# Kernel optimization log

Measured on AMD Instinct MI355X. Metric: run time of the kernel, lower is better.

## Reference

```python
import jax, jax.numpy as jnp
import numpy as np

D_MODEL = 1024
NUM_HEADS = 16
HEAD_DIM = D_MODEL // NUM_HEADS  # 64
ROPE_BASE = 10000.0


def _rope_tables(n_pos, dim):
    # 1D rotary tables for `dim` channels (rotate-half convention).
    inv_freq = 1.0 / (ROPE_BASE ** (jnp.arange(0, dim, 2, dtype=jnp.float32) / dim))
    ang = jnp.arange(n_pos, dtype=jnp.float32)[:, None] * inv_freq[None, :]  # (P, dim/2)
    cos = jnp.concatenate([jnp.cos(ang), jnp.cos(ang)], axis=-1)  # (P, dim)
    sin = jnp.concatenate([jnp.sin(ang), jnp.sin(ang)], axis=-1)
    return cos, sin


def _rotate_half(v):
    v1, v2 = jnp.split(v, 2, axis=-1)
    return jnp.concatenate([-v2, v1], axis=-1)


def rope_2d(x, H, W):
    # x: (N, H, W, nh, hd). First half of hd rotated by row index, second by col index.
    d_half = HEAD_DIM // 2
    x_h, x_w = x[..., :d_half], x[..., d_half:]
    cos_h, sin_h = _rope_tables(H, d_half)  # (H, d_half)
    cos_w, sin_w = _rope_tables(W, d_half)  # (W, d_half)
    cos_h = cos_h[None, :, None, None, :]
    sin_h = sin_h[None, :, None, None, :]
    cos_w = cos_w[None, None, :, None, :]
    sin_w = sin_w[None, None, :, None, :]
    x_h = x_h * cos_h + _rotate_half(x_h) * sin_h
    x_w = x_w * cos_w + _rotate_half(x_w) * sin_w
    return jnp.concatenate([x_h, x_w], axis=-1)


def setup_inputs() -> dict:
    key = jax.random.key(0)
    k_x, k_qkv, k_p, k_b = jax.random.split(key, 4)
    B, T, H, W = 4, 32, 16, 16
    x = jax.random.normal(k_x, (B, T, H, W, D_MODEL), dtype=jnp.float32)
    w_qkv = jax.random.normal(k_qkv, (D_MODEL, 3 * D_MODEL), dtype=jnp.float32) * 0.02
    w_proj = jax.random.normal(k_p, (D_MODEL, D_MODEL), dtype=jnp.float32) * 0.02
    b_proj = jax.random.normal(k_b, (D_MODEL,), dtype=jnp.float32) * 0.02
    return {"x": x, "w_qkv": w_qkv, "w_proj": w_proj, "b_proj": b_proj}


def reference(x, w_qkv, w_proj, b_proj):
    B, T, H, W, C = x.shape
    N, S = B * T, H * W
    scale = HEAD_DIM ** -0.5
    xf = x.reshape(N, S, C)
    qkv = xf @ w_qkv  # (N, S, 3C)  [qkv_bias=False]
    q, k, v = jnp.split(qkv, 3, axis=-1)
    q = q.reshape(N, H, W, NUM_HEADS, HEAD_DIM)
    k = k.reshape(N, H, W, NUM_HEADS, HEAD_DIM)
    v = v.reshape(N, S, NUM_HEADS, HEAD_DIM)
    q = rope_2d(q, H, W).reshape(N, S, NUM_HEADS, HEAD_DIM)
    k = rope_2d(k, H, W).reshape(N, S, NUM_HEADS, HEAD_DIM)
    attn = jnp.einsum('nshd,nthd->nhst', q, k) * scale  # (N, nh, S, S)
    attn = jax.nn.softmax(attn, axis=-1)  # attn_drop=0.0
    out = jnp.einsum('nhst,nthd->nshd', attn, v).reshape(N, S, C)
    out = out @ w_proj + b_proj
    return out.reshape(B, T, H, W, C)
```

## Files before the change

kernel.cpp:

```cpp
#include <hip/hip_runtime.h>
#include <hip/hip_bf16.h>
#include <stdint.h>

typedef __attribute__((ext_vector_type(8))) short bf16x8;
typedef __attribute__((ext_vector_type(4))) float f32x4;
typedef __attribute__((ext_vector_type(4))) unsigned short ushort4_t;

__device__ __forceinline__ unsigned short f2bf(float f) {
  union { float f; unsigned int i; } x; x.f = f;
  return (unsigned short)((x.i + 0x7fffu + ((x.i >> 16) & 1u)) >> 16);
}

__device__ __forceinline__ void gl_lds16(const void* g, void* l) {
  __builtin_amdgcn_global_load_lds(
      (const __attribute__((address_space(1))) unsigned int*)(uintptr_t)g,
      (__attribute__((address_space(3))) unsigned int*)(uint32_t)(uintptr_t)l,
      16, 0, 0);
}

__device__ __forceinline__ void bar() {
  asm volatile("" ::: "memory");
  __builtin_amdgcn_s_barrier();
  asm volatile("" ::: "memory");
}

__constant__ float INVF[16] = {
  1.0f,   0.56234132519f,  0.31622776601f,  0.17782794100f,
  0.1f,   0.056234132519f, 0.031622776601f, 0.017782794100f,
  0.01f,  0.0056234132519f,0.0031622776601f,0.0017782794100f,
  0.001f, 0.00056234132519f,0.00031622776601f,0.00017782794100f
};

__global__ __launch_bounds__(256) void k_conv_x(const float4* __restrict__ src,
                                                ushort4_t* __restrict__ dst, int n4) {
  int i = blockIdx.x * 256 + threadIdx.x;
  if (i < n4) {
    float4 v = src[i];
    ushort4_t r = { f2bf(v.x), f2bf(v.y), f2bf(v.z), f2bf(v.w) };
    dst[i] = r;
  }
}

__global__ __launch_bounds__(256) void k_transpose_bf16(const float* __restrict__ src,
                                                        unsigned short* __restrict__ dst,
                                                        int R, int C) {
  __shared__ unsigned short tile[64][65];
  const int bj = blockIdx.x, bi = blockIdx.y;
  const int t = threadIdx.x, lr = t >> 6, lc = t & 63;
  #pragma unroll
  for (int i = 0; i < 16; i++) {
    int r = i * 4 + lr;
    tile[r][lc] = f2bf(src[(size_t)(bi * 64 + r) * C + bj * 64 + lc]);
  }
  __syncthreads();
  #pragma unroll
  for (int i = 0; i < 16; i++) {
    int r = i * 4 + lr;
    dst[(size_t)(bj * 64 + r) * R + bi * 64 + lc] = tile[lc][r];
  }
}

template<int F32OUT, int ROPE>
__global__ __launch_bounds__(512, 2) void k_gemm_bt(
    const unsigned short* __restrict__ A, const unsigned short* __restrict__ B,
    unsigned short* __restrict__ Cb, float* __restrict__ Cf,
    const float* __restrict__ bias, int M, int N, int K) {
  __shared__ __align__(16) unsigned short As[2 * 256 * 64];
  __shared__ __align__(16) unsigned short Bs[2 * 256 * 64];
  const int tid = threadIdx.x;
  const int lane = tid & 63, wid = tid >> 6;
  const int cl = lane & 15, gr = lane >> 4;
  const int wm = wid >> 2, wn = wid & 3;
  const int l8 = lane >> 3, l7 = lane & 7;
  const int mBase = blockIdx.y * 256, nBase = blockIdx.x * 256;
  const int KT = K >> 6;
  const int ldsW = (wid * 8) * 64;

  const unsigned short* aP[4];
  const unsigned short* bP[4];
  #pragma unroll
  for (int i = 0; i < 4; i++) {
    aP[i] = A + (size_t)(mBase + i * 64 + wid * 8 + l8) * K + (l7 ^ l8) * 8;
    bP[i] = B + (size_t)(nBase + i * 64 + wid * 8 + l8) * K + (l7 ^ l8) * 8;
  }

  const f32x4 zero4 = {0.f, 0.f, 0.f, 0.f};
  f32x4 acc[8][4];
  #pragma unroll
  for (int a = 0; a < 8; a++)
    #pragma unroll
    for (int b = 0; b < 4; b++) acc[a][b] = zero4;

  #pragma unroll
  for (int i = 0; i < 4; i++) gl_lds16(aP[i], &As[(i * 64) * 64 + ldsW]);
  #pragma unroll
  for (int i = 0; i < 4; i++) gl_lds16(bP[i], &Bs[(i * 64) * 64 + ldsW]);
  #pragma unroll
  for (int i = 0; i < 4; i++) gl_lds16(aP[i] + 64, &As[16384 + (i * 64) * 64 + ldsW]);
  #pragma unroll
  for (int i = 0; i < 4; i++) gl_lds16(bP[i] + 64, &Bs[16384 + (i * 64) * 64 + ldsW]);
  asm volatile("s_waitcnt vmcnt(8)" ::: "memory");
  bar();

  for (int c = 0; c < KT; ++c) {
    const int s = c & 1;
    const unsigned short* as_ = As + s * 16384;
    const unsigned short* bs_ = Bs + s * 16384;

    if (c + 1 < KT) {
      const int koff = (c + 1) * 64;
      const int so = (s ^ 1) * 16384;
      #pragma unroll
      for (int i = 0; i < 4; i++) gl_lds16(aP[i] + koff, &As[so + (i * 64) * 64 + ldsW]);
      #pragma unroll
      for (int i = 0; i < 4; i++) gl_lds16(bP[i] + koff, &Bs[so + (i * 64) * 64 + ldsW]);
    }

    #pragma unroll
    for (int kc = 0; kc < 2; ++kc) {
      const int coff = ((kc * 4 + gr) ^ (cl & 7)) * 8;
      bf16x8 bv[4];
      #pragma unroll
      for (int nt = 0; nt < 4; nt++)
        bv[nt] = *(const bf16x8*)&bs_[(wn * 64 + nt * 16 + cl) * 64 + coff];
      #pragma unroll
      for (int h = 0; h < 2; ++h) {
        bf16x8 af[4];
        #pragma unroll
        for (int t = 0; t < 4; t++)
          af[t] = *(const bf16x8*)&as_[(wm * 128 + h * 64 + t * 16 + cl) * 64 + coff];
        __builtin_amdgcn_s_setprio(1);
        #pragma unroll
        for (int mt = 0; mt < 4; mt++)
          #pragma unroll
          for (int nt = 0; nt < 4; nt++)
            acc[h * 4 + mt][nt] =
                __builtin_amdgcn_mfma_f32_16x16x32_bf16(af[mt], bv[nt], acc[h * 4 + mt][nt], 0, 0, 0);
        __builtin_amdgcn_s_setprio(0);
      }
    }

    if (c + 1 < KT) {
      asm volatile("s_waitcnt vmcnt(0)" ::: "memory");
      bar();
    }
  }

  if (ROPE && nBase < 2048) {
    const float f = INVF[cl];
    #pragma unroll
    for (int amt = 0; amt < 8; amt++)
      #pragma unroll
      for (int r = 0; r < 4; r++) {
        const int sp = (mBase + wm * 128 + amt * 16 + gr * 4 + r) & 255;
        float sh, ch, sw, cw;
        __sincosf((float)(sp >> 4) * f, &sh, &ch);
        __sincosf((float)(sp & 15) * f, &sw, &cw);
        const float a = acc[amt][0][r], b = acc[amt][1][r];
        const float cc = acc[amt][2][r], d = acc[amt][3][r];
        acc[amt][0][r] = a * ch - b * sh;
        acc[amt][1][r] = b * ch + a * sh;
        acc[amt][2][r] = cc * cw - d * sw;
        acc[amt][3][r] = d * cw + cc * sw;
      }
  }

  #pragma unroll
  for (int amt = 0; amt < 8; amt++)
    #pragma unroll
    for (int nt = 0; nt < 4; nt++)
      #pragma unroll
      for (int r = 0; r < 4; r++) {
        const int row = mBase + wm * 128 + amt * 16 + gr * 4 + r;
        const int col = nBase + wn * 64 + nt * 16 + cl;
        const float v = acc[amt][nt][r];
        if (F32OUT) Cf[(size_t)row * N + col] = v + bias[col];
        else        Cb[(size_t)row * N + col] = f2bf(v);
      }
}

__global__ __launch_bounds__(256, 3) void k_attn(const unsigned short* __restrict__ qkv,
                                                 unsigned short* __restrict__ attn_out) {
  __shared__ __align__(16) unsigned short Qp[4][64 * 64];
  __shared__ __align__(16) unsigned short Kt[64 * 64];
  __shared__ __align__(16) unsigned short Vt[64 * 64];
  const int blk = blockIdx.x;
  const int n = blk >> 4, h = blk & 15;
  const int tid = threadIdx.x;
  const int lane = tid & 63, wid = tid >> 6;
  const int cl = lane & 15, gr = lane >> 4;
  const int l8 = lane >> 3, l7 = lane & 7;
  const unsigned short* qbase = qkv + (size_t)n * 256 * 3072 + h * 64;
  const unsigned short* kbase = qbase + 1024;
  const unsigned short* vbase = qbase + 2048;

  #pragma unroll
  for (int i = 0; i < 8; i++)
    gl_lds16(qbase + (size_t)(wid * 64 + i * 8 + l8) * 3072 + (l7 ^ l8) * 8,
             &Qp[wid][i * 8 * 64]);
  #pragma unroll
  for (int i = 0; i < 2; i++) {
    const int r0 = (wid * 2 + i) * 8;
    gl_lds16(kbase + (size_t)(r0 + l8) * 3072 + (l7 ^ l8) * 8, &Kt[r0 * 64]);
  }

  unsigned int vr[2][4];
  #pragma unroll
  for (int i = 0; i < 2; i++) {
    const int u = i * 256 + tid;
    const int t0 = u >> 5, d = (u & 31) * 2;
    #pragma unroll
    for (int k = 0; k < 4; k++)
      vr[i][k] = *(const unsigned int*)(vbase + (size_t)(t0 + 16 * k) * 3072 + d);
  }
  __syncthreads();

  bf16x8 qf[4][2];
  #pragma unroll
  for (int mt = 0; mt < 4; mt++)
    #pragma unroll
    for (int kc = 0; kc < 2; kc++)
      qf[mt][kc] = *(const bf16x8*)&Qp[wid][(mt * 16 + cl) * 64 + ((kc * 4 + gr) ^ (cl & 7)) * 8];

  const f32x4 zero4 = {0.f, 0.f, 0.f, 0.f};
  f32x4 o[4][4];
  float lsum[4][4];
  #pragma unroll
  for (int a = 0; a < 4; a++)
    #pragma unroll
    for (int b = 0; b < 4; b++) { o[a][b] = zero4; lsum[a][b] = 0.f; }

  for (int tc = 0; tc < 4; tc++) {
    #pragma unroll
    for (int i = 0; i < 2; i++) {
      const int u = i * 256 + tid;
      const int t0 = u >> 5, d = (u & 31) * 2;
      const unsigned int r0 = vr[i][0], r1 = vr[i][1], r2 = vr[i][2], r3 = vr[i][3];
      uint2 lo, hi;
      lo.x = (r0 & 0xffffu) | (r1 << 16);
      lo.y = (r2 & 0xffffu) | (r3 << 16);
      hi.x = (r0 >> 16) | (r1 & 0xffff0000u);
      hi.y = (r2 >> 16) | (r3 & 0xffff0000u);
      *(uint2*)&Vt[d * 64 + ((t0 >> 1) ^ (d & 7)) * 8 + (t0 & 1) * 4] = lo;
      const int d1 = d + 1;
      *(uint2*)&Vt[d1 * 64 + ((t0 >> 1) ^ (d1 & 7)) * 8 + (t0 & 1) * 4] = hi;
    }
    if (tc < 3) {
      #pragma unroll
      for (int i = 0; i < 2; i++) {
        const int u = i * 256 + tid;
        const int t0 = u >> 5, d = (u & 31) * 2;
        #pragma unroll
        for (int k = 0; k < 4; k++)
          vr[i][k] = *(const unsigned int*)(vbase + (size_t)((tc + 1) * 64 + t0 + 16 * k) * 3072 + d);
      }
    }

    #pragma unroll
    for (int mt = 0; mt < 4; mt++) {
      f32x4 sacc[4] = {zero4, zero4, zero4, zero4};
      #pragma unroll
      for (int kc = 0; kc < 2; kc++)
        #pragma unroll
        for (int nt = 0; nt < 4; nt++) {
          const bf16x8 kf = *(const bf16x8*)&Kt[(nt * 16 + cl) * 64 + ((kc * 4 + gr) ^ (cl & 7)) * 8];
          sacc[nt] = __builtin_amdgcn_mfma_f32_16x16x32_bf16(qf[mt][kc], kf, sacc[nt], 0, 0, 0);
        }
      #pragma unroll
      for (int r = 0; r < 4; r++) {
        const float p0 = __expf(sacc[0][r] * 0.125f);
        const float p1 = __expf(sacc[1][r] * 0.125f);
        const float p2 = __expf(sacc[2][r] * 0.125f);
        const float p3 = __expf(sacc[3][r] * 0.125f);
        lsum[mt][r] += (p0 + p1) + (p2 + p3);
        float2 f01; f01.x = p0; f01.y = p1;
        float2 f23; f23.x = p2; f23.y = p3;
        __hip_bfloat162 b01 = __float22bfloat162_rn(f01);
        __hip_bfloat162 b23 = __float22bfloat162_rn(f23);
        union { __hip_bfloat162 h; unsigned int u; } c0, c1;
        c0.h = b01; c1.h = b23;
        uint2 w; w.x = c0.u; w.y = c1.u;
        const int m = mt * 16 + gr * 4 + r;
        *(uint2*)&Qp[wid][m * 64 + ((cl >> 1) ^ (m & 7)) * 8 + (cl & 1) * 4] = w;
      }
    }
    __syncthreads();

    if (tc < 3) {
      #pragma unroll
      for (int i = 0; i < 2; i++) {
        const int r0 = (wid * 2 + i) * 8;
        gl_lds16(kbase + (size_t)((tc + 1) * 64 + r0 + l8) * 3072 + (l7 ^ l8) * 8, &Kt[r0 * 64]);
      }
    }

    #pragma unroll
    for (int kc = 0; kc < 2; kc++) {
      bf16x8 vf[4], pf[4];
      #pragma unroll
      for (int dt = 0; dt < 4; dt++)
        vf[dt] = *(const bf16x8*)&Vt[(dt * 16 + cl) * 64 + ((kc * 4 + gr) ^ (cl & 7)) * 8];
      #pragma unroll
      for (int mt = 0; mt < 4; mt++)
        pf[mt] = *(const bf16x8*)&Qp[wid][(mt * 16 + cl) * 64 + ((kc * 4 + gr) ^ (cl & 7)) * 8];
      #pragma unroll
      for (int mt = 0; mt < 4; mt++)
        #pragma unroll
        for (int dt = 0; dt < 4; dt++)
          o[mt][dt] = __builtin_amdgcn_mfma_f32_16x16x32_bf16(pf[mt], vf[dt], o[mt][dt], 0, 0, 0);
    }
    __syncthreads();
  }

  #pragma unroll
  for (int mt = 0; mt < 4; mt++)
    #pragma unroll
    for (int r = 0; r < 4; r++) {
      float l = lsum[mt][r];
      l += __shfl_xor(l, 1);
      l += __shfl_xor(l, 2);
      l += __shfl_xor(l, 4);
      l += __shfl_xor(l, 8);
      const float inv = 1.0f / l;
      const int srow = wid * 64 + mt * 16 + gr * 4 + r;
      #pragma unroll
      for (int dt = 0; dt < 4; dt++)
        attn_out[(size_t)(n * 256 + srow) * 1024 + h * 64 + dt * 16 + cl] =
            f2bf(o[mt][dt][r] * inv);
    }
}

extern "C" void kernel_launch(void* const* d_in, const int* in_sizes, int n_in,
                              void* d_out, int out_size, void* d_ws, size_t ws_size,
                              hipStream_t stream) {
  const float* x      = (const float*)d_in[0];
  const float* w_qkv  = (const float*)d_in[1];
  const float* w_proj = (const float*)d_in[2];
  const float* b_proj = (const float*)d_in[3];
  float* out = (float*)d_out;
  char* ws = (char*)d_ws;

  unsigned short* x_bf    = (unsigned short*)ws;
  unsigned short* wqkvT   = (unsigned short*)(ws + 67108864);
  unsigned short* wprojT  = (unsigned short*)(ws + 73400320);
  unsigned short* qkvb    = (unsigned short*)(ws + 75497472);
  unsigned short* attn_bf = x_bf;

  k_conv_x<<<32768, 256, 0, stream>>>((const float4*)x, (ushort4_t*)x_bf, 8388608);
  k_transpose_bf16<<<dim3(48, 16), 256, 0, stream>>>(w_qkv, wqkvT, 1024, 3072);
  k_transpose_bf16<<<dim3(16, 16), 256, 0, stream>>>(w_proj, wprojT, 1024, 1024);

  k_gemm_bt<0, 1><<<dim3(12, 128), 512, 0, stream>>>(x_bf, wqkvT, qkvb, nullptr, nullptr,
                                                     32768, 3072, 1024);
  k_attn<<<2048, 256, 0, stream>>>(qkvb, attn_bf);

  k_gemm_bt<1, 0><<<dim3(4, 128), 512, 0, stream>>>(attn_bf, wprojT, nullptr, out, b_proj,
                                                    32768, 1024, 1024);
}
```

Measured before the change: 657.2 us.

## Restructure GEMM main loop into quadrant-staged ping-pong pipeline with XCD-aware block remap

```diff
diff --git a/kernel.cpp b/kernel.cpp
--- a/kernel.cpp
+++ b/kernel.cpp
@@ -59,6 +59,55 @@
     dst[(size_t)(bj * 64 + r) * R + bi * 64 + lc] = tile[lc][r];
   }
 }
+
+
+#define LDA(dst, base, hm)                                                      \
+  do {                                                                          \
+    _Pragma("unroll") for (int t_ = 0; t_ < 4; t_++) {                          \
+      dst[0][t_] = *(const bf16x8*)&base[(wm * 128 + (hm) * 64 + t_ * 16 + cl) * 64 + cf0]; \
+      dst[1][t_] = *(const bf16x8*)&base[(wm * 128 + (hm) * 64 + t_ * 16 + cl) * 64 + cf1]; \
+    }                                                                           \
+  } while (0)
+
+#define LDB(dst, base, hn)                                                      \
+  do {                                                                          \
+    _Pragma("unroll") for (int u_ = 0; u_ < 2; u_++) {                          \
+      dst[0][u_] = *(const bf16x8*)&base[(wn * 64 + (hn) * 32 + u_ * 16 + cl) * 64 + cf0]; \
+      dst[1][u_] = *(const bf16x8*)&base[(wn * 64 + (hn) * 32 + u_ * 16 + cl) * 64 + cf1]; \
+    }                                                                           \
+  } while (0)
+
+#define MFMA_Q(hm, hn, AFR, BVR)                                                \
+  do {                                                                          \
+    __builtin_amdgcn_s_setprio(1);                                              \
+    _Pragma("unroll") for (int kc_ = 0; kc_ < 2; kc_++)                         \
+      _Pragma("unroll") for (int mt_ = 0; mt_ < 4; mt_++)                       \
+        _Pragma("unroll") for (int u_ = 0; u_ < 2; u_++)                        \
+          acc[(hm) * 4 + mt_][(hn) * 2 + u_] =                                  \
+              __builtin_amdgcn_mfma_f32_16x16x32_bf16(                          \
+                  AFR[kc_][mt_], BVR[kc_][u_],                                  \
+                  acc[(hm) * 4 + mt_][(hn) * 2 + u_], 0, 0, 0);                 \
+    __builtin_amdgcn_s_setprio(0);                                              \
+  } while (0)
+
+#define STAGE_A(tile_, half_)                                                   \
+  do {                                                                          \
+    const int so_ = ((tile_) & 1) * 16384;                                      \
+    const int ko_ = (tile_) * 64;                                               \
+    gl_lds16(aP[(half_) * 2] + ko_,     &As[so_ + ((half_) * 2) * 4096 + ldsW]);     \
+    gl_lds16(aP[(half_) * 2 + 1] + ko_, &As[so_ + ((half_) * 2 + 1) * 4096 + ldsW]); \
+  } while (0)
+
+#define STAGE_B(tile_, half_)                                                   \
+  do {                                                                          \
+    const int so_ = ((tile_) & 1) * 16384;                                      \
+    const int ko_ = (tile_) * 64;                                               \
+    gl_lds16(bP[(half_) * 2] + ko_,     &Bs[so_ + ((half_) * 2) * 4096 + ldsW]);     \
+    gl_lds16(bP[(half_) * 2 + 1] + ko_, &Bs[so_ + ((half_) * 2 + 1) * 4096 + ldsW]); \
+  } while (0)
+
+#define LGKM0() asm volatile("s_waitcnt lgkmcnt(0)" ::: "memory")
+#define VMC(n)  asm volatile("s_waitcnt vmcnt(" #n ")" ::: "memory")
 
 template<int F32OUT, int ROPE>
 __global__ __launch_bounds__(512, 2) void k_gemm_bt(
@@ -72,9 +121,19 @@
   const int cl = lane & 15, gr = lane >> 4;
   const int wm = wid >> 2, wn = wid & 3;
   const int l8 = lane >> 3, l7 = lane & 7;
-  const int mBase = blockIdx.y * 256, nBase = blockIdx.x * 256;
+
+  const int gx = gridDim.x;
+  const int nwg = gx * gridDim.y;
+  const int fb = blockIdx.y * gx + blockIdx.x;
+  const int q = nwg >> 3;
+  const int nid = (fb & 7) * q + (fb >> 3);
+  const int bx = nid % gx, by = nid / gx;
+  const int mBase = by * 256, nBase = bx * 256;
+
   const int KT = K >> 6;
   const int ldsW = (wid * 8) * 64;
+  const int cf0 = ((0 * 4 + gr) ^ (cl & 7)) * 8;
+  const int cf1 = ((1 * 4 + gr) ^ (cl & 7)) * 8;
 
   const unsigned short* aP[4];
   const unsigned short* bP[4];
@@ -91,71 +150,74 @@
     #pragma unroll
     for (int b = 0; b < 4; b++) acc[a][b] = zero4;
 
-  #pragma unroll
-  for (int i = 0; i < 4; i++) gl_lds16(aP[i], &As[(i * 64) * 64 + ldsW]);
-  #pragma unroll
-  for (int i = 0; i < 4; i++) gl_lds16(bP[i], &Bs[(i * 64) * 64 + ldsW]);
-  #pragma unroll
-  for (int i = 0; i < 4; i++) gl_lds16(aP[i] + 64, &As[16384 + (i * 64) * 64 + ldsW]);
-  #pragma unroll
-  for (int i = 0; i < 4; i++) gl_lds16(bP[i] + 64, &Bs[16384 + (i * 64) * 64 + ldsW]);
-  asm volatile("s_waitcnt vmcnt(8)" ::: "memory");
+  STAGE_A(0, 0); STAGE_A(0, 1); STAGE_B(0, 0); STAGE_B(0, 1);
+  STAGE_B(1, 0); STAGE_B(1, 1);
+  VMC(4);
   bar();
 
-  for (int c = 0; c < KT; ++c) {
-    const int s = c & 1;
-    const unsigned short* as_ = As + s * 16384;
-    const unsigned short* bs_ = Bs + s * 16384;
-
-    if (c + 1 < KT) {
-      const int koff = (c + 1) * 64;
-      const int so = (s ^ 1) * 16384;
-      #pragma unroll
-      for (int i = 0; i < 4; i++) gl_lds16(aP[i] + koff, &As[so + (i * 64) * 64 + ldsW]);
-      #pragma unroll
-      for (int i = 0; i < 4; i++) gl_lds16(bP[i] + koff, &Bs[so + (i * 64) * 64 + ldsW]);
-    }
-
-    #pragma unroll
-    for (int kc = 0; kc < 2; ++kc) {
-      const int coff = ((kc * 4 + gr) ^ (cl & 7)) * 8;
-      bf16x8 bv[4];
-      #pragma unroll
-      for (int nt = 0; nt < 4; nt++)
-        bv[nt] = *(const bf16x8*)&bs_[(wn * 64 + nt * 16 + cl) * 64 + coff];
-      #pragma unroll
-      for (int h = 0; h < 2; ++h) {
-        bf16x8 af[4];
-        #pragma unroll
-        for (int t = 0; t < 4; t++)
-          af[t] = *(const bf16x8*)&as_[(wm * 128 + h * 64 + t * 16 + cl) * 64 + coff];
-        __builtin_amdgcn_s_setprio(1);
-        #pragma unroll
-        for (int mt = 0; mt < 4; mt++)
-          #pragma unroll
-          for (int nt = 0; nt < 4; nt++)
-            acc[h * 4 + mt][nt] =
-                __builtin_amdgcn_mfma_f32_16x16x32_bf16(af[mt], bv[nt], acc[h * 4 + mt][nt], 0, 0, 0);
-        __builtin_amdgcn_s_setprio(0);
-      }
-    }
-
-    if (c + 1 < KT) {
-      asm volatile("s_waitcnt vmcnt(0)" ::: "memory");
-      bar();
-    }
+  bf16x8 af[2][4], bva[2][2], bvb[2][2];
+
+  for (int c = 0; c < KT; c += 2) {
+    const unsigned short* a0 = As;
+    const unsigned short* b0 = Bs;
+    const unsigned short* a1 = As + 16384;
+    const unsigned short* b1 = Bs + 16384;
+    const int c2 = c + 2, c3 = c + 3;
+
+    LDA(af, a0, 0); LDB(bva, b0, 0);
+    STAGE_A(c + 1, 0);
+    asm volatile("s_waitcnt lgkmcnt(8)" ::: "memory");
+    bar(); LGKM0();
+    MFMA_Q(0, 0, af, bva);
+    bar();
+    LDB(bvb, b0, 1);
+    STAGE_A(c + 1, 1);
+    bar(); LGKM0();
+    MFMA_Q(0, 1, af, bvb);
+    bar();
+    LDA(af, a0, 1);
+    if (c2 < KT) STAGE_B(c2, 0);
+    bar(); LGKM0();
+    MFMA_Q(1, 1, af, bvb);
+    bar();
+    if (c2 < KT) { STAGE_B(c2, 1); VMC(4); } else { VMC(0); }
+    bar();
+    MFMA_Q(1, 0, af, bva);
+    bar();
+
+    LDA(af, a1, 0); LDB(bva, b1, 0);
+    if (c2 < KT) STAGE_A(c2, 0);
+    asm volatile("s_waitcnt lgkmcnt(8)" ::: "memory");
+    bar(); LGKM0();
+    MFMA_Q(0, 0, af, bva);
+    bar();
+    LDB(bvb, b1, 1);
+    if (c2 < KT) STAGE_A(c2, 1);
+    bar(); LGKM0();
+    MFMA_Q(0, 1, af, bvb);
+    bar();
+    LDA(af, a1, 1);
+    if (c3 < KT) STAGE_B(c3, 0);
+    bar(); LGKM0();
+    MFMA_Q(1, 1, af, bvb);
+    bar();
+    if (c3 < KT)      { STAGE_B(c3, 1); VMC(4); }
+    else if (c2 < KT) { VMC(0); }
+    bar();
+    MFMA_Q(1, 0, af, bva);
+    if (c2 < KT) bar();
   }
 
   if (ROPE && nBase < 2048) {
-    const float f = INVF[cl];
+    const float f2 = INVF[cl];
     #pragma unroll
     for (int amt = 0; amt < 8; amt++)
       #pragma unroll
       for (int r = 0; r < 4; r++) {
         const int sp = (mBase + wm * 128 + amt * 16 + gr * 4 + r) & 255;
         float sh, ch, sw, cw;
-        __sincosf((float)(sp >> 4) * f, &sh, &ch);
-        __sincosf((float)(sp & 15) * f, &sw, &cw);
+        __sincosf((float)(sp >> 4) * f2, &sh, &ch);
+        __sincosf((float)(sp & 15) * f2, &sw, &cw);
         const float a = acc[amt][0][r], b = acc[amt][1][r];
         const float cc = acc[amt][2][r], d = acc[amt][3][r];
         acc[amt][0][r] = a * ch - b * sh;
```

New measurement: 640.8 us. 2.5% less time.
